# Kernel tuning notes

Hardware: AMD Instinct MI355X
Metric: run time of the kernel (lower is better)

The kernel has to match this reference:

```python
import jax, jax.numpy as jnp
import numpy as np

NUM_NODES = 100000
NUM_EDGES = 1600000
IN_DIM = 128
HID = 128
OUT_DIM = 5


def setup_inputs() -> dict:
    key = jax.random.key(0)
    ks = jax.random.split(key, 8)
    x = jax.random.normal(ks[0], (NUM_NODES, IN_DIM), dtype=jnp.float32)
    edges = jax.random.randint(ks[1], (2, NUM_EDGES), 0, NUM_NODES, dtype=jnp.int32)
    s = 1.0 / np.sqrt(IN_DIM)
    W1 = jax.random.uniform(ks[2], (IN_DIM, HID), jnp.float32, -s, s)
    b1 = jax.random.uniform(ks[3], (HID,), jnp.float32, -s, s)
    sh = 1.0 / np.sqrt(HID)
    W2 = jax.random.uniform(ks[4], (HID, HID), jnp.float32, -sh, sh)
    b2 = jax.random.uniform(ks[5], (HID,), jnp.float32, -sh, sh)
    Wp = jax.random.uniform(ks[6], (HID, OUT_DIM), jnp.float32, -sh, sh)
    bp = jax.random.uniform(ks[7], (OUT_DIM,), jnp.float32, -sh, sh)
    return {"x": x, "edges": edges, "W1": W1, "b1": b1, "W2": W2, "b2": b2, "Wp": Wp, "bp": bp}


def _gnn_layer(x, src, tgt, W, b):
    # scatter-add of source features into targets (mean aggregation)
    agg = jax.ops.segment_sum(x[src], tgt, num_segments=NUM_NODES)  # [N, d]
    cnt = jax.ops.segment_sum(jnp.ones_like(tgt, dtype=x.dtype), tgt, num_segments=NUM_NODES)
    cnt = jnp.maximum(cnt, 1.0)  # clamp(min=1)
    agg = agg / cnt[:, None]
    combined = x + agg  # residual
    return jax.nn.relu(combined @ W + b)


def reference(x, edges, W1, b1, W2, b2, Wp, bp):
    src, tgt = edges[0], edges[1]
    h = _gnn_layer(x, src, tgt, W1, b1)
    h = _gnn_layer(h, src, tgt, W2, b2)
    return h @ Wp + bp  # [N, OUT_DIM]
```

## Files before the change

kernel.cpp:

```cpp
#include <hip/hip_runtime.h>

typedef unsigned int uint32;
typedef unsigned short ushort16;

typedef __attribute__((ext_vector_type(8))) short short8;
typedef __attribute__((ext_vector_type(4))) float f32x4;


#define RSH 11
#define NRG 2048
#define CAP 49152
#define CH  2048

__device__ __forceinline__ ushort16 f2bf(float f) {
    uint32 u = __float_as_uint(f);
    u += 0x7fffu + ((u >> 16) & 1u);
    return (ushort16)(u >> 16);
}
__device__ __forceinline__ float bfhi(uint32 u) { return __uint_as_float(u & 0xffff0000u); }
__device__ __forceinline__ float bflo(uint32 u) { return __uint_as_float(u << 16); }
__device__ __forceinline__ uint32 pack2(float a, float b) {
    return (uint32)f2bf(a) | ((uint32)f2bf(b) << 16);
}

union U16 { uint4 u; short8 s; };
__device__ __forceinline__ short8 ld_frag(const ushort16* p) {
    U16 x; x.u = *(const uint4*)p; return x.s;
}

#define ACC8(v) \
    acc[0] += bflo(v.x); acc[1] += bfhi(v.x); \
    acc[2] += bflo(v.y); acc[3] += bfhi(v.y); \
    acc[4] += bflo(v.z); acc[5] += bfhi(v.z); \
    acc[6] += bflo(v.w); acc[7] += bfhi(v.w);

__global__ __launch_bounds__(256)
void count_prep_kernel(const int* __restrict__ tgt, int* __restrict__ hist,
                       const float* __restrict__ W1, const float* __restrict__ W2,
                       ushort16* __restrict__ Wt1, ushort16* __restrict__ Wt2,
                       int E, int PB, int R) {
    int tid = threadIdx.x, blk = blockIdx.x;
    if (blk >= PB) {
        int idx = blk - PB;
        const float* W = (idx >> 3) ? W2 : W1;
        ushort16* Wt = (idx >> 3) ? Wt2 : Wt1;
        int i0 = (idx & 7) * 2048 + tid * 8;
        float4 a = *(const float4*)(W + i0);
        float4 b = *(const float4*)(W + i0 + 4);
        int k = i0 >> 7, col = i0 & 127;
        Wt[(col + 0) * 128 + k] = f2bf(a.x);
        Wt[(col + 1) * 128 + k] = f2bf(a.y);
        Wt[(col + 2) * 128 + k] = f2bf(a.z);
        Wt[(col + 3) * 128 + k] = f2bf(a.w);
        Wt[(col + 4) * 128 + k] = f2bf(b.x);
        Wt[(col + 5) * 128 + k] = f2bf(b.y);
        Wt[(col + 6) * 128 + k] = f2bf(b.z);
        Wt[(col + 7) * 128 + k] = f2bf(b.w);
        return;
    }
    __shared__ int cnt[64];
    if (tid < 64) cnt[tid] = 0;
    __syncthreads();
    int q0 = blk * (CH / 4), q1 = min(q0 + CH / 4, E / 4);
    for (int q = q0 + tid; q < q1; q += 256) {
        int4 t = ((const int4*)tgt)[q];
        atomicAdd(&cnt[t.x >> RSH], 1);
        atomicAdd(&cnt[t.y >> RSH], 1);
        atomicAdd(&cnt[t.z >> RSH], 1);
        atomicAdd(&cnt[t.w >> RSH], 1);
    }
    __syncthreads();
    if (tid < R) hist[(size_t)blk * 64 + tid] = cnt[tid];
}

__global__ __launch_bounds__(256)
void scan_kernel(int* __restrict__ hist, int* __restrict__ total, int PB) {
    __shared__ int sd[256];
    __shared__ int carrySh;
    int r = blockIdx.x, tid = threadIdx.x;
    if (tid == 0) carrySh = 0;
    __syncthreads();
    int chunks = (PB + 255) >> 8;
    for (int ch = 0; ch < chunks; ++ch) {
        int g = ch * 256 + tid;
        int v = (g < PB) ? hist[(size_t)g * 64 + r] : 0;
        int c0 = carrySh;
        sd[tid] = v;
        __syncthreads();
        for (int o = 1; o < 256; o <<= 1) {
            int t = (tid >= o) ? sd[tid - o] : 0;
            __syncthreads();
            sd[tid] += t;
            __syncthreads();
        }
        if (g < PB) hist[(size_t)g * 64 + r] = sd[tid] - v + c0;
        int tot = sd[255];
        __syncthreads();
        if (tid == 0) carrySh = c0 + tot;
        __syncthreads();
    }
    if (tid == 0) total[r] = carrySh;
}

__global__ __launch_bounds__(256)
void scatter_kernel(const int* __restrict__ src, const int* __restrict__ tgt,
                    const int* __restrict__ hist, uint2* __restrict__ rlist,
                    int E, int R) {
    __shared__ int cb[64];
    __shared__ int cnt[64];
    int tid = threadIdx.x, blk = blockIdx.x;
    if (tid < 64) {
        cnt[tid] = 0;
        cb[tid] = (tid < R) ? hist[(size_t)blk * 64 + tid] : 0;
    }
    __syncthreads();
    int q0 = blk * (CH / 4), q1 = min(q0 + CH / 4, E / 4);
    for (int q = q0 + tid; q < q1; q += 256) {
        int4 t = ((const int4*)tgt)[q];
        int4 s = ((const int4*)src)[q];
        int r0 = t.x >> RSH, r1 = t.y >> RSH, r2 = t.z >> RSH, r3 = t.w >> RSH;
        int l0 = atomicAdd(&cnt[r0], 1);
        int l1 = atomicAdd(&cnt[r1], 1);
        int l2 = atomicAdd(&cnt[r2], 1);
        int l3 = atomicAdd(&cnt[r3], 1);
        int p0 = cb[r0] + l0, p1 = cb[r1] + l1, p2 = cb[r2] + l2, p3 = cb[r3] + l3;
        if (p0 < CAP) rlist[(size_t)r0 * CAP + p0] = make_uint2((uint32)s.x, (uint32)t.x);
        if (p1 < CAP) rlist[(size_t)r1 * CAP + p1] = make_uint2((uint32)s.y, (uint32)t.y);
        if (p2 < CAP) rlist[(size_t)r2 * CAP + p2] = make_uint2((uint32)s.z, (uint32)t.z);
        if (p3 < CAP) rlist[(size_t)r3 * CAP + p3] = make_uint2((uint32)s.w, (uint32)t.w);
    }
}

template<int INF32>
__device__ __forceinline__
void gemm_rows(const void* __restrict__ Asrc, const ushort16* __restrict__ Wt,
               int M, ushort16* __restrict__ outB, int r0w) {
    const int lane = threadIdx.x & 63;
    const int l15 = lane & 15;
    const int quad = lane >> 4;

    int arow = r0w + l15;
    if (arow >= M) arow = M - 1;

    short8 afr[4];
    if (INF32) {
        const float* ap = (const float*)Asrc + (size_t)arow * 128 + quad * 8;
#pragma unroll
        for (int kt = 0; kt < 4; ++kt) {
            float4 a0 = *(const float4*)(ap + kt * 32);
            float4 a1 = *(const float4*)(ap + kt * 32 + 4);
            short8 f;
            f[0] = (short)f2bf(a0.x); f[1] = (short)f2bf(a0.y);
            f[2] = (short)f2bf(a0.z); f[3] = (short)f2bf(a0.w);
            f[4] = (short)f2bf(a1.x); f[5] = (short)f2bf(a1.y);
            f[6] = (short)f2bf(a1.z); f[7] = (short)f2bf(a1.w);
            afr[kt] = f;
        }
    } else {
        const ushort16* aptr = (const ushort16*)Asrc + (size_t)arow * 128 + quad * 8;
#pragma unroll
        for (int kt = 0; kt < 4; ++kt) afr[kt] = ld_frag(aptr + kt * 32);
    }

    f32x4 acc[8];
#pragma unroll
    for (int t = 0; t < 8; ++t) acc[t] = (f32x4){0.f, 0.f, 0.f, 0.f};

#pragma unroll
    for (int t = 0; t < 8; ++t) {
        const ushort16* bptr = Wt + (size_t)(16 * t + l15) * 128 + quad * 8;
        short8 b0 = ld_frag(bptr);
        short8 b1 = ld_frag(bptr + 32);
        short8 b2 = ld_frag(bptr + 64);
        short8 b3 = ld_frag(bptr + 96);
        acc[t] = __builtin_amdgcn_mfma_f32_16x16x32_bf16(afr[0], b0, acc[t], 0, 0, 0);
        acc[t] = __builtin_amdgcn_mfma_f32_16x16x32_bf16(afr[1], b1, acc[t], 0, 0, 0);
        acc[t] = __builtin_amdgcn_mfma_f32_16x16x32_bf16(afr[2], b2, acc[t], 0, 0, 0);
        acc[t] = __builtin_amdgcn_mfma_f32_16x16x32_bf16(afr[3], b3, acc[t], 0, 0, 0);
    }

#pragma unroll
    for (int t = 0; t < 8; ++t) {
        float ov[4];
        ov[0] = acc[t].x; ov[1] = acc[t].y; ov[2] = acc[t].z; ov[3] = acc[t].w;
#pragma unroll
        for (int r = 0; r < 4; ++r) {
            float nb = __shfl_xor(ov[r], 1, 64);
            int row = r0w + quad * 4 + r;
            if (((l15 & 1) == 0) && row < M) {
                *(uint32*)(outB + (size_t)row * 128 + 16 * t + l15) = pack2(ov[r], nb);
            }
        }
    }
}

__global__ __launch_bounds__(1024)
void csr_gemm1_kernel(const uint2* __restrict__ rlist, const int* __restrict__ total,
                      int* __restrict__ start, int* __restrict__ deg,
                      int* __restrict__ csr, int N, int R,
                      const float* __restrict__ x, const ushort16* __restrict__ Wt1,
                      ushort16* __restrict__ ybuf) {
    int blk = blockIdx.x;
    int tid = threadIdx.x;
    if (blk >= R) {
        int gid = blk - R;
        gemm_rows<1>(x, Wt1, N, ybuf, gid * 256 + (tid >> 6) * 16);
        return;
    }
    __shared__ int hist[NRG];
    __shared__ int sd[1024];
    __shared__ int carrySh;
    __shared__ int rbaseSh, countSh;

    int r = blk;
    if (tid == 0) countSh = min(total[r], CAP);
    if (tid < 64) {
        int v = (tid < R) ? total[tid] : 0;
        int pm = (tid < r) ? v : 0;
#pragma unroll
        for (int o = 1; o < 64; o <<= 1) pm += __shfl_xor(pm, o, 64);
        if (tid == 0) rbaseSh = pm;
    }
    for (int i = tid; i < NRG; i += 1024) hist[i] = 0;
    __syncthreads();
    int count = countSh;
    const uint2* rl = rlist + (size_t)r * CAP;
    int n0 = r << RSH;

    {
        int i = tid;
        for (; i + 3072 < count; i += 4096) {
            uint2 a = rl[i], b = rl[i + 1024], c = rl[i + 2048], d = rl[i + 3072];
            atomicAdd(&hist[a.y & (NRG - 1)], 1);
            atomicAdd(&hist[b.y & (NRG - 1)], 1);
            atomicAdd(&hist[c.y & (NRG - 1)], 1);
            atomicAdd(&hist[d.y & (NRG - 1)], 1);
        }
        for (; i < count; i += 1024)
            atomicAdd(&hist[rl[i].y & (NRG - 1)], 1);
    }
    __syncthreads();

    if (tid == 0) carrySh = rbaseSh;
    __syncthreads();
    for (int ch = 0; ch < 2; ++ch) {
        int idx = ch * 1024 + tid;
        int v = hist[idx];
        int c0 = carrySh;
        sd[tid] = v;
        __syncthreads();
        for (int o = 1; o < 1024; o <<= 1) {
            int t = (tid >= o) ? sd[tid - o] : 0;
            __syncthreads();
            sd[tid] += t;
            __syncthreads();
        }
        int excl = sd[tid] - v + c0;
        int tot = sd[1023];
        int node = n0 + idx;
        if (node < N) { start[node] = excl; deg[node] = v; }
        __syncthreads();
        hist[idx] = excl;
        if (tid == 0) carrySh = c0 + tot;
        __syncthreads();
    }

    {
        int i = tid;
        for (; i + 3072 < count; i += 4096) {
            uint2 a = rl[i], b = rl[i + 1024], c = rl[i + 2048], d = rl[i + 3072];
            int pa = atomicAdd(&hist[a.y & (NRG - 1)], 1);
            int pb = atomicAdd(&hist[b.y & (NRG - 1)], 1);
            int pc = atomicAdd(&hist[c.y & (NRG - 1)], 1);
            int pd = atomicAdd(&hist[d.y & (NRG - 1)], 1);
            csr[pa] = (int)a.x;
            csr[pb] = (int)b.x;
            csr[pc] = (int)c.x;
            csr[pd] = (int)d.x;
        }
        for (; i < count; i += 1024) {
            uint2 e = rl[i];
            int p = atomicAdd(&hist[e.y & (NRG - 1)], 1);
            csr[p] = (int)e.x;
        }
    }
}

template<int INF32>
__global__ __launch_bounds__(256)
void gemm_raw_kernel(const void* __restrict__ Asrc, const ushort16* __restrict__ Wt,
                     int M, ushort16* __restrict__ outB) {
    gemm_rows<INF32>(Asrc, Wt, M, outB, blockIdx.x * 64 + (threadIdx.x >> 6) * 16);
}

template<int PROJ>
__global__ __launch_bounds__(256, 4)
void agg_fuse_kernel(const ushort16* __restrict__ hb,
                     const int* __restrict__ start, const int* __restrict__ degv,
                     const int* __restrict__ csr,
                     const float* __restrict__ bias,
                     uint32* __restrict__ outb,
                     const float* __restrict__ Wp, const float* __restrict__ bp,
                     float* __restrict__ outP, int N) {
    int wid = (blockIdx.x * 256 + threadIdx.x) >> 6;
    int lane = threadIdx.x & 63;
    if (wid >= N) return;
    int g = lane >> 4, sl = lane & 15;
    int s0 = start[wid];
    int deg = degv[wid];
    int fi = sl * 4 + g;
    uint32 su = ((const uint32*)hb)[(size_t)wid * 64 + fi];

    float acc[8];
#pragma unroll
    for (int j = 0; j < 8; ++j) acc[j] = 0.f;

    int base = 0;
    for (; base + 8 <= deg; base += 8) {
        int i0 = csr[s0 + base + g];
        int i1 = csr[s0 + base + 4 + g];
        uint4 v0 = *(const uint4*)(hb + (size_t)i0 * 128 + sl * 8);
        uint4 v1 = *(const uint4*)(hb + (size_t)i1 * 128 + sl * 8);
        ACC8(v0); ACC8(v1);
    }
    for (; base < deg; base += 4) {
        int e = base + g;
        if (e < deg) {
            int s = csr[s0 + e];
            uint4 v = *(const uint4*)(hb + (size_t)s * 128 + sl * 8);
            ACC8(v);
        }
    }
#pragma unroll
    for (int j = 0; j < 8; ++j) {
        acc[j] += __shfl_xor(acc[j], 16, 64);
        acc[j] += __shfl_xor(acc[j], 32, 64);
    }
    float inv = 1.f / fmaxf((float)deg, 1.f);
    float ax = (g == 0) ? acc[0] : (g == 1) ? acc[2] : (g == 2) ? acc[4] : acc[6];
    float ay = (g == 0) ? acc[1] : (g == 1) ? acc[3] : (g == 2) ? acc[5] : acc[7];

    float ha = fmaxf(bflo(su) + ax * inv + bias[2 * fi],     0.f);
    float hc = fmaxf(bfhi(su) + ay * inv + bias[2 * fi + 1], 0.f);

    if (!PROJ) {
        outb[(size_t)wid * 64 + fi] = pack2(ha, hc);
    } else {
        float p[5];
#pragma unroll
        for (int j = 0; j < 5; ++j)
            p[j] = ha * Wp[(2 * fi) * 5 + j] + hc * Wp[(2 * fi + 1) * 5 + j];
#pragma unroll
        for (int m = 1; m <= 32; m <<= 1)
#pragma unroll
            for (int j = 0; j < 5; ++j) p[j] += __shfl_xor(p[j], m, 64);
        if (lane == 0) {
#pragma unroll
            for (int j = 0; j < 5; ++j) outP[(size_t)wid * 5 + j] = p[j] + bp[j];
        }
    }
}

extern "C" void kernel_launch(void* const* d_in, const int* in_sizes, int n_in,
                              void* d_out, int out_size, void* d_ws, size_t ws_size,
                              hipStream_t stream) {
    const float* x     = (const float*)d_in[0];
    const int*   edges = (const int*)d_in[1];
    const float* W1    = (const float*)d_in[2];
    const float* b1    = (const float*)d_in[3];
    const float* W2    = (const float*)d_in[4];
    const float* b2    = (const float*)d_in[5];
    const float* Wp    = (const float*)d_in[6];
    const float* bp    = (const float*)d_in[7];
    float* out = (float*)d_out;

    int N = in_sizes[0] / 128;
    int E = in_sizes[1] / 2;
    const int* src = edges;
    const int* tgt = edges + E;

    const int R  = (N + NRG - 1) >> RSH;
    const int PB = (E + CH - 1) / CH;

    char* ws = (char*)d_ws;
    size_t off = 0;
    auto alloc = [&](size_t bytes) {
        char* p = ws + off;
        off = (off + bytes + 255) & ~(size_t)255;
        return p;
    };
    int*      deg     = (int*)alloc((size_t)N * 4);
    int*      start   = (int*)alloc((size_t)N * 4);
    int*      csr     = (int*)alloc((size_t)E * 4);
    uint2*    rlist   = (uint2*)alloc((size_t)R * CAP * 8);
    int*      hist    = (int*)alloc((size_t)PB * 64 * 4);
    int*      total   = (int*)alloc(64 * 4);
    ushort16* ybuf    = (ushort16*)alloc((size_t)N * 128 * 2);
    ushort16* h1      = (ushort16*)alloc((size_t)N * 128 * 2);
    ushort16* Wt1     = (ushort16*)alloc(128 * 128 * 2);
    ushort16* Wt2     = (ushort16*)alloc(128 * 128 * 2);
    (void)ws_size;

    const int g1Blocks   = (N + 255) / 256;
    const int gemmBlocks = (N + 63) / 64;
    const int aggBlocks  = (N + 3) / 4;

    count_prep_kernel<<<PB + 16, 256, 0, stream>>>(tgt, hist, W1, W2, Wt1, Wt2,
                                                   E, PB, R);
    scan_kernel<<<R, 256, 0, stream>>>(hist, total, PB);
    scatter_kernel<<<PB, 256, 0, stream>>>(src, tgt, hist, rlist, E, R);
    csr_gemm1_kernel<<<R + g1Blocks, 1024, 0, stream>>>(rlist, total, start, deg,
                                                        csr, N, R, x, Wt1, ybuf);
    agg_fuse_kernel<0><<<aggBlocks, 256, 0, stream>>>(ybuf, start, deg, csr, b1,
                                                      (uint32*)h1, nullptr, nullptr,
                                                      nullptr, N);
    gemm_raw_kernel<0><<<gemmBlocks, 256, 0, stream>>>(h1, Wt2, N, ybuf);
    agg_fuse_kernel<1><<<aggBlocks, 256, 0, stream>>>(ybuf, start, deg, csr, b2,
                                                      nullptr, Wp, bp, out, N);
}
```

Baseline: 325.3 us.

## Fuse edge partition count/scan/scatter into one kernel with atomic cursors

Replaces the three-kernel partition pipeline (per-block histogram, global scan, scatter) with one kernel. Each block counts its edges in shared memory, reserves space per range through a global atomic cursor, then scatters. This drops two launches and the hist round trip. Bucket ranges shrink to 1024 nodes (up to 128 ranges), so the CSR build now scans one chunk, and nontemporal loads and stores are used throughout. In exchange, edge order inside each range is no longer deterministic, and smaller buckets give more, smaller work units.

```diff
diff --git a/kernel.cpp b/kernel.cpp
--- a/kernel.cpp
+++ b/kernel.cpp
@@ -5,11 +5,14 @@
 
 typedef __attribute__((ext_vector_type(8))) short short8;
 typedef __attribute__((ext_vector_type(4))) float f32x4;
-
-
-#define RSH 11
-#define NRG 2048
-#define CAP 49152
+typedef __attribute__((ext_vector_type(4))) int i32x4;
+typedef __attribute__((ext_vector_type(2))) uint32 u32x2;
+typedef __attribute__((ext_vector_type(4))) uint32 u32x4;
+
+
+#define RSH 10
+#define NRG 1024
+#define CAP 24576
 #define CH  2048
 
 __device__ __forceinline__ ushort16 f2bf(float f) {
@@ -26,6 +29,10 @@
 union U16 { uint4 u; short8 s; };
 __device__ __forceinline__ short8 ld_frag(const ushort16* p) {
     U16 x; x.u = *(const uint4*)p; return x.s;
+}
+union U16NT { u32x4 u; short8 s; };
+__device__ __forceinline__ short8 ld_frag_nt(const ushort16* p) {
+    U16NT x; x.u = __builtin_nontemporal_load((const u32x4*)p); return x.s;
 }
 
 #define ACC8(v) \
@@ -35,10 +42,11 @@
     acc[6] += bflo(v.w); acc[7] += bfhi(v.w);
 
 __global__ __launch_bounds__(256)
-void count_prep_kernel(const int* __restrict__ tgt, int* __restrict__ hist,
-                       const float* __restrict__ W1, const float* __restrict__ W2,
-                       ushort16* __restrict__ Wt1, ushort16* __restrict__ Wt2,
-                       int E, int PB, int R) {
+void partition_prep_kernel(const int* __restrict__ src, const int* __restrict__ tgt,
+                           uint2* __restrict__ rlist, int* __restrict__ rcursor,
+                           const float* __restrict__ W1, const float* __restrict__ W2,
+                           ushort16* __restrict__ Wt1, ushort16* __restrict__ Wt2,
+                           int E, int PB, int R) {
     int tid = threadIdx.x, blk = blockIdx.x;
     if (blk >= PB) {
         int idx = blk - PB;
@@ -58,76 +66,48 @@
         Wt[(col + 7) * 128 + k] = f2bf(b.w);
         return;
     }
-    __shared__ int cnt[64];
-    if (tid < 64) cnt[tid] = 0;
+    __shared__ int cnt[128];
+    __shared__ int cbase[128];
+    if (tid < 128) cnt[tid] = 0;
     __syncthreads();
     int q0 = blk * (CH / 4), q1 = min(q0 + CH / 4, E / 4);
     for (int q = q0 + tid; q < q1; q += 256) {
-        int4 t = ((const int4*)tgt)[q];
+        i32x4 t = __builtin_nontemporal_load((const i32x4*)tgt + q);
         atomicAdd(&cnt[t.x >> RSH], 1);
         atomicAdd(&cnt[t.y >> RSH], 1);
         atomicAdd(&cnt[t.z >> RSH], 1);
         atomicAdd(&cnt[t.w >> RSH], 1);
     }
-    __syncthreads();
-    if (tid < R) hist[(size_t)blk * 64 + tid] = cnt[tid];
-}
-
-__global__ __launch_bounds__(256)
-void scan_kernel(int* __restrict__ hist, int* __restrict__ total, int PB) {
-    __shared__ int sd[256];
-    __shared__ int carrySh;
-    int r = blockIdx.x, tid = threadIdx.x;
-    if (tid == 0) carrySh = 0;
-    __syncthreads();
-    int chunks = (PB + 255) >> 8;
-    for (int ch = 0; ch < chunks; ++ch) {
-        int g = ch * 256 + tid;
-        int v = (g < PB) ? hist[(size_t)g * 64 + r] : 0;
-        int c0 = carrySh;
-        sd[tid] = v;
-        __syncthreads();
-        for (int o = 1; o < 256; o <<= 1) {
-            int t = (tid >= o) ? sd[tid - o] : 0;
-            __syncthreads();
-            sd[tid] += t;
-            __syncthreads();
-        }
-        if (g < PB) hist[(size_t)g * 64 + r] = sd[tid] - v + c0;
-        int tot = sd[255];
-        __syncthreads();
-        if (tid == 0) carrySh = c0 + tot;
-        __syncthreads();
-    }
-    if (tid == 0) total[r] = carrySh;
-}
-
-__global__ __launch_bounds__(256)
-void scatter_kernel(const int* __restrict__ src, const int* __restrict__ tgt,
-                    const int* __restrict__ hist, uint2* __restrict__ rlist,
-                    int E, int R) {
-    __shared__ int cb[64];
-    __shared__ int cnt[64];
-    int tid = threadIdx.x, blk = blockIdx.x;
-    if (tid < 64) {
-        cnt[tid] = 0;
-        cb[tid] = (tid < R) ? hist[(size_t)blk * 64 + tid] : 0;
-    }
-    __syncthreads();
-    int q0 = blk * (CH / 4), q1 = min(q0 + CH / 4, E / 4);
+    if (blk == 0 && tid == 0)
+        for (int e = (E / 4) * 4; e < E; ++e) atomicAdd(&cnt[tgt[e] >> RSH], 1);
+    __syncthreads();
+    if (tid < R) cbase[tid] = atomicAdd(&rcursor[tid], cnt[tid]);
+    __syncthreads();
+    if (tid < 128) cnt[tid] = 0;
+    __syncthreads();
     for (int q = q0 + tid; q < q1; q += 256) {
-        int4 t = ((const int4*)tgt)[q];
-        int4 s = ((const int4*)src)[q];
+        i32x4 t = __builtin_nontemporal_load((const i32x4*)tgt + q);
+        i32x4 s = __builtin_nontemporal_load((const i32x4*)src + q);
         int r0 = t.x >> RSH, r1 = t.y >> RSH, r2 = t.z >> RSH, r3 = t.w >> RSH;
-        int l0 = atomicAdd(&cnt[r0], 1);
-        int l1 = atomicAdd(&cnt[r1], 1);
-        int l2 = atomicAdd(&cnt[r2], 1);
-        int l3 = atomicAdd(&cnt[r3], 1);
-        int p0 = cb[r0] + l0, p1 = cb[r1] + l1, p2 = cb[r2] + l2, p3 = cb[r3] + l3;
-        if (p0 < CAP) rlist[(size_t)r0 * CAP + p0] = make_uint2((uint32)s.x, (uint32)t.x);
-        if (p1 < CAP) rlist[(size_t)r1 * CAP + p1] = make_uint2((uint32)s.y, (uint32)t.y);
-        if (p2 < CAP) rlist[(size_t)r2 * CAP + p2] = make_uint2((uint32)s.z, (uint32)t.z);
-        if (p3 < CAP) rlist[(size_t)r3 * CAP + p3] = make_uint2((uint32)s.w, (uint32)t.w);
+        int p0 = cbase[r0] + atomicAdd(&cnt[r0], 1);
+        int p1 = cbase[r1] + atomicAdd(&cnt[r1], 1);
+        int p2 = cbase[r2] + atomicAdd(&cnt[r2], 1);
+        int p3 = cbase[r3] + atomicAdd(&cnt[r3], 1);
+        u32x2 e0; e0.x = (uint32)s.x; e0.y = (uint32)t.x;
+        u32x2 e1; e1.x = (uint32)s.y; e1.y = (uint32)t.y;
+        u32x2 e2; e2.x = (uint32)s.z; e2.y = (uint32)t.z;
+        u32x2 e3; e3.x = (uint32)s.w; e3.y = (uint32)t.w;
+        if (p0 < CAP) __builtin_nontemporal_store(e0, (u32x2*)&rlist[(size_t)r0 * CAP + p0]);
+        if (p1 < CAP) __builtin_nontemporal_store(e1, (u32x2*)&rlist[(size_t)r1 * CAP + p1]);
+        if (p2 < CAP) __builtin_nontemporal_store(e2, (u32x2*)&rlist[(size_t)r2 * CAP + p2]);
+        if (p3 < CAP) __builtin_nontemporal_store(e3, (u32x2*)&rlist[(size_t)r3 * CAP + p3]);
+    }
+    if (blk == 0 && tid == 0) {
+        for (int e = (E / 4) * 4; e < E; ++e) {
+            int t = tgt[e], r = t >> RSH;
+            int p = cbase[r] + atomicAdd(&cnt[r], 1);
+            if (p < CAP) rlist[(size_t)r * CAP + p] = make_uint2((uint32)src[e], (uint32)t);
+        }
     }
 }
 
@@ -147,8 +127,8 @@
         const float* ap = (const float*)Asrc + (size_t)arow * 128 + quad * 8;
 #pragma unroll
         for (int kt = 0; kt < 4; ++kt) {
-            float4 a0 = *(const float4*)(ap + kt * 32);
-            float4 a1 = *(const float4*)(ap + kt * 32 + 4);
+            f32x4 a0 = __builtin_nontemporal_load((const f32x4*)(ap + kt * 32));
+            f32x4 a1 = __builtin_nontemporal_load((const f32x4*)(ap + kt * 32 + 4));
             short8 f;
             f[0] = (short)f2bf(a0.x); f[1] = (short)f2bf(a0.y);
             f[2] = (short)f2bf(a0.z); f[3] = (short)f2bf(a0.w);
@@ -159,7 +139,7 @@
     } else {
         const ushort16* aptr = (const ushort16*)Asrc + (size_t)arow * 128 + quad * 8;
 #pragma unroll
-        for (int kt = 0; kt < 4; ++kt) afr[kt] = ld_frag(aptr + kt * 32);
+        for (int kt = 0; kt < 4; ++kt) afr[kt] = ld_frag_nt(aptr + kt * 32);
     }
 
     f32x4 acc[8];
@@ -188,14 +168,15 @@
             float nb = __shfl_xor(ov[r], 1, 64);
             int row = r0w + quad * 4 + r;
             if (((l15 & 1) == 0) && row < M) {
-                *(uint32*)(outB + (size_t)row * 128 + 16 * t + l15) = pack2(ov[r], nb);
+                __builtin_nontemporal_store(pack2(ov[r], nb),
+                    (uint32*)(outB + (size_t)row * 128 + 16 * t + l15));
             }
         }
     }
 }
 
 __global__ __launch_bounds__(1024)
-void csr_gemm1_kernel(const uint2* __restrict__ rlist, const int* __restrict__ total,
+void csr_gemm1_kernel(const uint2* __restrict__ rlist, const int* __restrict__ rcursor,
                       int* __restrict__ start, int* __restrict__ deg,
                       int* __restrict__ csr, int N, int R,
                       const float* __restrict__ x, const ushort16* __restrict__ Wt1,
@@ -209,44 +190,50 @@
     }
     __shared__ int hist[NRG];
     __shared__ int sd[1024];
-    __shared__ int carrySh;
     __shared__ int rbaseSh, countSh;
 
     int r = blk;
-    if (tid == 0) countSh = min(total[r], CAP);
-    if (tid < 64) {
-        int v = (tid < R) ? total[tid] : 0;
-        int pm = (tid < r) ? v : 0;
-#pragma unroll
-        for (int o = 1; o < 64; o <<= 1) pm += __shfl_xor(pm, o, 64);
-        if (tid == 0) rbaseSh = pm;
-    }
-    for (int i = tid; i < NRG; i += 1024) hist[i] = 0;
+    if (tid < 128) sd[tid] = (tid < R) ? rcursor[tid] : 0;
+    __syncthreads();
+    for (int o = 1; o < 128; o <<= 1) {
+        int t = (tid >= o && tid < 128) ? sd[tid - o] : 0;
+        __syncthreads();
+        if (tid < 128) sd[tid] += t;
+        __syncthreads();
+    }
+    if (tid == 0) {
+        int incl = sd[r];
+        int excl = (r == 0) ? 0 : sd[r - 1];
+        rbaseSh = excl;
+        countSh = min(incl - excl, CAP);
+    }
+    hist[tid] = 0;
     __syncthreads();
     int count = countSh;
-    const uint2* rl = rlist + (size_t)r * CAP;
+    const u32x2* rl = (const u32x2*)(rlist + (size_t)r * CAP);
     int n0 = r << RSH;
 
     {
         int i = tid;
         for (; i + 3072 < count; i += 4096) {
-            uint2 a = rl[i], b = rl[i + 1024], c = rl[i + 2048], d = rl[i + 3072];
+            u32x2 a = __builtin_nontemporal_load(rl + i);
+            u32x2 b = __builtin_nontemporal_load(rl + i + 1024);
+            u32x2 c = __builtin_nontemporal_load(rl + i + 2048);
+            u32x2 d = __builtin_nontemporal_load(rl + i + 3072);
             atomicAdd(&hist[a.y & (NRG - 1)], 1);
             atomicAdd(&hist[b.y & (NRG - 1)], 1);
             atomicAdd(&hist[c.y & (NRG - 1)], 1);
             atomicAdd(&hist[d.y & (NRG - 1)], 1);
         }
-        for (; i < count; i += 1024)
-            atomicAdd(&hist[rl[i].y & (NRG - 1)], 1);
-    }
-    __syncthreads();
-
-    if (tid == 0) carrySh = rbaseSh;
-    __syncthreads();
-    for (int ch = 0; ch < 2; ++ch) {
-        int idx = ch * 1024 + tid;
-        int v = hist[idx];
-        int c0 = carrySh;
+        for (; i < count; i += 1024) {
+            u32x2 e = __builtin_nontemporal_load(rl + i);
+            atomicAdd(&hist[e.y & (NRG - 1)], 1);
+        }
+    }
+    __syncthreads();
+
+    {
+        int v = hist[tid];
         sd[tid] = v;
         __syncthreads();
         for (int o = 1; o < 1024; o <<= 1) {
@@ -255,33 +242,33 @@
             sd[tid] += t;
             __syncthreads();
         }
-        int excl = sd[tid] - v + c0;
-        int tot = sd[1023];
-        int node = n0 + idx;
+        int excl = sd[tid] - v + rbaseSh;
+        int node = n0 + tid;
         if (node < N) { start[node] = excl; deg[node] = v; }
-        __syncthreads();
-        hist[idx] = excl;
-        if (tid == 0) carrySh = c0 + tot;
+        hist[tid] = excl;
         __syncthreads();
     }
 
     {
         int i = tid;
         for (; i + 3072 < count; i += 4096) {
-            uint2 a = rl[i], b = rl[i + 1024], c = rl[i + 2048], d = rl[i + 3072];
+            u32x2 a = __builtin_nontemporal_load(rl + i);
+            u32x2 b = __builtin_nontemporal_load(rl + i + 1024);
+            u32x2 c = __builtin_nontemporal_load(rl + i + 2048);
+            u32x2 d = __builtin_nontemporal_load(rl + i + 3072);
             int pa = atomicAdd(&hist[a.y & (NRG - 1)], 1);
             int pb = atomicAdd(&hist[b.y & (NRG - 1)], 1);
             int pc = atomicAdd(&hist[c.y & (NRG - 1)], 1);
             int pd = atomicAdd(&hist[d.y & (NRG - 1)], 1);
-            csr[pa] = (int)a.x;
-            csr[pb] = (int)b.x;
-            csr[pc] = (int)c.x;
-            csr[pd] = (int)d.x;
+            __builtin_nontemporal_store((int)a.x, &csr[pa]);
+            __builtin_nontemporal_store((int)b.x, &csr[pb]);
+            __builtin_nontemporal_store((int)c.x, &csr[pc]);
+            __builtin_nontemporal_store((int)d.x, &csr[pd]);
         }
         for (; i < count; i += 1024) {
-            uint2 e = rl[i];
+            u32x2 e = __builtin_nontemporal_load(rl + i);
             int p = atomicAdd(&hist[e.y & (NRG - 1)], 1);
-            csr[p] = (int)e.x;
+            __builtin_nontemporal_store((int)e.x, &csr[p]);
         }
     }
 }
@@ -344,7 +331,7 @@
     float hc = fmaxf(bfhi(su) + ay * inv + bias[2 * fi + 1], 0.f);
 
     if (!PROJ) {
-        outb[(size_t)wid * 64 + fi] = pack2(ha, hc);
+        __builtin_nontemporal_store(pack2(ha, hc), &outb[(size_t)wid * 64 + fi]);
     } else {
         float p[5];
 #pragma unroll
@@ -356,7 +343,8 @@
             for (int j = 0; j < 5; ++j) p[j] += __shfl_xor(p[j], m, 64);
         if (lane == 0) {
 #pragma unroll
-            for (int j = 0; j < 5; ++j) outP[(size_t)wid * 5 + j] = p[j] + bp[j];
+            for (int j = 0; j < 5; ++j)
+                __builtin_nontemporal_store(p[j] + bp[j], &outP[(size_t)wid * 5 + j]);
         }
     }
 }
@@ -393,8 +381,7 @@
     int*      start   = (int*)alloc((size_t)N * 4);
     int*      csr     = (int*)alloc((size_t)E * 4);
     uint2*    rlist   = (uint2*)alloc((size_t)R * CAP * 8);
-    int*      hist    = (int*)alloc((size_t)PB * 64 * 4);
-    int*      total   = (int*)alloc(64 * 4);
+    int*      rcursor = (int*)alloc(128 * 4);
     ushort16* ybuf    = (ushort16*)alloc((size_t)N * 128 * 2);
     ushort16* h1      = (ushort16*)alloc((size_t)N * 128 * 2);
     ushort16* Wt1     = (ushort16*)alloc(128 * 128 * 2);
@@ -405,11 +392,10 @@
     const int gemmBlocks = (N + 63) / 64;
     const int aggBlocks  = (N + 3) / 4;
 
-    count_prep_kernel<<<PB + 16, 256, 0, stream>>>(tgt, hist, W1, W2, Wt1, Wt2,
-                                                   E, PB, R);
-    scan_kernel<<<R, 256, 0, stream>>>(hist, total, PB);
-    scatter_kernel<<<PB, 256, 0, stream>>>(src, tgt, hist, rlist, E, R);
-    csr_gemm1_kernel<<<R + g1Blocks, 1024, 0, stream>>>(rlist, total, start, deg,
+    (void)hipMemsetAsync(rcursor, 0, 128 * 4, stream);
+    partition_prep_kernel<<<PB + 16, 256, 0, stream>>>(src, tgt, rlist, rcursor,
+                                                       W1, W2, Wt1, Wt2, E, PB, R);
+    csr_gemm1_kernel<<<R + g1Blocks, 1024, 0, stream>>>(rlist, rcursor, start, deg,
                                                         csr, N, R, x, Wt1, ybuf);
     agg_fuse_kernel<0><<<aggBlocks, 256, 0, stream>>>(ybuf, start, deg, csr, b1,
                                                       (uint32*)h1, nullptr, nullptr,
```

New measurement: 412.8 us. 1.27x slower.

## Move bias+ReLU into next GEMM and split projection into separate kernel

Applied to the files above, without the earlier changes.

The aggregation kernel now only writes the bf16 residual-plus-mean sum, without bias, ReLU or projection. Layer-1 bias and ReLU are applied while loading A fragments in the second GEMM, and a new per-node projection kernel applies layer-2 bias, ReLU and the 128x5 projection, reading Wp from shared memory. This removes the cross-lane shuffle reductions from the aggregation, at the cost of one extra launch and an extra N×128 bf16 read/write. The change also adds tail handling for edge counts not divisible by four and moves rlist to the end of the workspace.

```diff
diff --git a/kernel.cpp b/kernel.cpp
--- a/kernel.cpp
+++ b/kernel.cpp
@@ -69,6 +69,8 @@
         atomicAdd(&cnt[t.z >> RSH], 1);
         atomicAdd(&cnt[t.w >> RSH], 1);
     }
+    if (blk == 0 && tid == 0)
+        for (int e = (E / 4) * 4; e < E; ++e) atomicAdd(&cnt[tgt[e] >> RSH], 1);
     __syncthreads();
     if (tid < R) hist[(size_t)blk * 64 + tid] = cnt[tid];
 }
@@ -119,22 +121,29 @@
         int4 t = ((const int4*)tgt)[q];
         int4 s = ((const int4*)src)[q];
         int r0 = t.x >> RSH, r1 = t.y >> RSH, r2 = t.z >> RSH, r3 = t.w >> RSH;
-        int l0 = atomicAdd(&cnt[r0], 1);
-        int l1 = atomicAdd(&cnt[r1], 1);
-        int l2 = atomicAdd(&cnt[r2], 1);
-        int l3 = atomicAdd(&cnt[r3], 1);
-        int p0 = cb[r0] + l0, p1 = cb[r1] + l1, p2 = cb[r2] + l2, p3 = cb[r3] + l3;
+        int p0 = cb[r0] + atomicAdd(&cnt[r0], 1);
+        int p1 = cb[r1] + atomicAdd(&cnt[r1], 1);
+        int p2 = cb[r2] + atomicAdd(&cnt[r2], 1);
+        int p3 = cb[r3] + atomicAdd(&cnt[r3], 1);
         if (p0 < CAP) rlist[(size_t)r0 * CAP + p0] = make_uint2((uint32)s.x, (uint32)t.x);
         if (p1 < CAP) rlist[(size_t)r1 * CAP + p1] = make_uint2((uint32)s.y, (uint32)t.y);
         if (p2 < CAP) rlist[(size_t)r2 * CAP + p2] = make_uint2((uint32)s.z, (uint32)t.z);
         if (p3 < CAP) rlist[(size_t)r3 * CAP + p3] = make_uint2((uint32)s.w, (uint32)t.w);
     }
-}
-
-template<int INF32>
+    if (blk == 0 && tid == 0) {
+        for (int e = (E / 4) * 4; e < E; ++e) {
+            int t = tgt[e], r = t >> RSH;
+            int p = cb[r] + atomicAdd(&cnt[r], 1);
+            if (p < CAP) rlist[(size_t)r * CAP + p] = make_uint2((uint32)src[e], (uint32)t);
+        }
+    }
+}
+
+template<int MODE>
 __device__ __forceinline__
 void gemm_rows(const void* __restrict__ Asrc, const ushort16* __restrict__ Wt,
-               int M, ushort16* __restrict__ outB, int r0w) {
+               const float* __restrict__ bias, int M,
+               ushort16* __restrict__ outB, int r0w) {
     const int lane = threadIdx.x & 63;
     const int l15 = lane & 15;
     const int quad = lane >> 4;
@@ -143,7 +152,7 @@
     if (arow >= M) arow = M - 1;
 
     short8 afr[4];
-    if (INF32) {
+    if (MODE == 1) {
         const float* ap = (const float*)Asrc + (size_t)arow * 128 + quad * 8;
 #pragma unroll
         for (int kt = 0; kt < 4; ++kt) {
@@ -155,6 +164,21 @@
             f[4] = (short)f2bf(a1.x); f[5] = (short)f2bf(a1.y);
             f[6] = (short)f2bf(a1.z); f[7] = (short)f2bf(a1.w);
             afr[kt] = f;
+        }
+    } else if (MODE == 2) {
+        const ushort16* aptr = (const ushort16*)Asrc + (size_t)arow * 128 + quad * 8;
+#pragma unroll
+        for (int kt = 0; kt < 4; ++kt) {
+            uint4 v = *(const uint4*)(aptr + kt * 32);
+            const float* bb = bias + kt * 32 + quad * 8;
+            float4 b0 = *(const float4*)bb;
+            float4 b1 = *(const float4*)(bb + 4);
+            uint32 w0 = pack2(fmaxf(bflo(v.x) + b0.x, 0.f), fmaxf(bfhi(v.x) + b0.y, 0.f));
+            uint32 w1 = pack2(fmaxf(bflo(v.y) + b0.z, 0.f), fmaxf(bfhi(v.y) + b0.w, 0.f));
+            uint32 w2 = pack2(fmaxf(bflo(v.z) + b1.x, 0.f), fmaxf(bfhi(v.z) + b1.y, 0.f));
+            uint32 w3 = pack2(fmaxf(bflo(v.w) + b1.z, 0.f), fmaxf(bfhi(v.w) + b1.w, 0.f));
+            U16 u; u.u = make_uint4(w0, w1, w2, w3);
+            afr[kt] = u.s;
         }
     } else {
         const ushort16* aptr = (const ushort16*)Asrc + (size_t)arow * 128 + quad * 8;
@@ -204,7 +228,7 @@
     int tid = threadIdx.x;
     if (blk >= R) {
         int gid = blk - R;
-        gemm_rows<1>(x, Wt1, N, ybuf, gid * 256 + (tid >> 6) * 16);
+        gemm_rows<1>(x, Wt1, nullptr, N, ybuf, gid * 256 + (tid >> 6) * 16);
         return;
     }
     __shared__ int hist[NRG];
@@ -286,27 +310,23 @@
     }
 }
 
-template<int INF32>
 __global__ __launch_bounds__(256)
-void gemm_raw_kernel(const void* __restrict__ Asrc, const ushort16* __restrict__ Wt,
-                     int M, ushort16* __restrict__ outB) {
-    gemm_rows<INF32>(Asrc, Wt, M, outB, blockIdx.x * 64 + (threadIdx.x >> 6) * 16);
-}
-
-template<int PROJ>
+void gemm_biasrelu_kernel(const ushort16* __restrict__ A, const ushort16* __restrict__ Wt,
+                          const float* __restrict__ bias, int M,
+                          ushort16* __restrict__ outB) {
+    gemm_rows<2>(A, Wt, bias, M, outB, blockIdx.x * 64 + ((threadIdx.x >> 6)) * 16);
+}
+
 __global__ __launch_bounds__(256, 4)
-void agg_fuse_kernel(const ushort16* __restrict__ hb,
-                     const int* __restrict__ start, const int* __restrict__ degv,
-                     const int* __restrict__ csr,
-                     const float* __restrict__ bias,
-                     uint32* __restrict__ outb,
-                     const float* __restrict__ Wp, const float* __restrict__ bp,
-                     float* __restrict__ outP, int N) {
+void agg_combine_bf16_kernel(const ushort16* __restrict__ hb,
+                             const int* __restrict__ startv, const int* __restrict__ degv,
+                             const int* __restrict__ csr,
+                             uint32* __restrict__ outb, int N) {
     int wid = (blockIdx.x * 256 + threadIdx.x) >> 6;
     int lane = threadIdx.x & 63;
     if (wid >= N) return;
     int g = lane >> 4, sl = lane & 15;
-    int s0 = start[wid];
+    int s0 = startv[wid];
     int deg = degv[wid];
     int fi = sl * 4 + g;
     uint32 su = ((const uint32*)hb)[(size_t)wid * 64 + fi];
@@ -339,26 +359,46 @@
     float inv = 1.f / fmaxf((float)deg, 1.f);
     float ax = (g == 0) ? acc[0] : (g == 1) ? acc[2] : (g == 2) ? acc[4] : acc[6];
     float ay = (g == 0) ? acc[1] : (g == 1) ? acc[3] : (g == 2) ? acc[5] : acc[7];
-
-    float ha = fmaxf(bflo(su) + ax * inv + bias[2 * fi],     0.f);
-    float hc = fmaxf(bfhi(su) + ay * inv + bias[2 * fi + 1], 0.f);
-
-    if (!PROJ) {
-        outb[(size_t)wid * 64 + fi] = pack2(ha, hc);
-    } else {
-        float p[5];
-#pragma unroll
-        for (int j = 0; j < 5; ++j)
-            p[j] = ha * Wp[(2 * fi) * 5 + j] + hc * Wp[(2 * fi + 1) * 5 + j];
-#pragma unroll
-        for (int m = 1; m <= 32; m <<= 1)
-#pragma unroll
-            for (int j = 0; j < 5; ++j) p[j] += __shfl_xor(p[j], m, 64);
-        if (lane == 0) {
-#pragma unroll
-            for (int j = 0; j < 5; ++j) outP[(size_t)wid * 5 + j] = p[j] + bp[j];
-        }
-    }
+    outb[(size_t)wid * 64 + fi] = pack2(bflo(su) + ax * inv, bfhi(su) + ay * inv);
+}
+
+__global__ __launch_bounds__(256)
+void proj_kernel(const ushort16* __restrict__ w, const float* __restrict__ b2,
+                 const float* __restrict__ Wp, const float* __restrict__ bp,
+                 float* __restrict__ out, int N) {
+    __shared__ float wps[640];
+    __shared__ float b2s[128];
+    int tid = threadIdx.x;
+    for (int i = tid; i < 640; i += 256) wps[i] = Wp[i];
+    if (tid < 128) b2s[tid] = b2[tid];
+    __syncthreads();
+    int n = blockIdx.x * 256 + tid;
+    if (n >= N) return;
+    const uint4* row = (const uint4*)(w + (size_t)n * 128);
+    float p0 = 0.f, p1 = 0.f, p2 = 0.f, p3 = 0.f, p4 = 0.f;
+#pragma unroll
+    for (int q = 0; q < 16; ++q) {
+        uint4 v = row[q];
+        int c = q * 8;
+        uint32 ww[4] = {v.x, v.y, v.z, v.w};
+#pragma unroll
+        for (int k = 0; k < 4; ++k) {
+            float hlo = fmaxf(bflo(ww[k]) + b2s[c + 2 * k],     0.f);
+            float hhi = fmaxf(bfhi(ww[k]) + b2s[c + 2 * k + 1], 0.f);
+            const float* wl = &wps[(c + 2 * k) * 5];
+            p0 += hlo * wl[0] + hhi * wl[5];
+            p1 += hlo * wl[1] + hhi * wl[6];
+            p2 += hlo * wl[2] + hhi * wl[7];
+            p3 += hlo * wl[3] + hhi * wl[8];
+            p4 += hlo * wl[4] + hhi * wl[9];
+        }
+    }
+    float* o = out + (size_t)n * 5;
+    o[0] = p0 + bp[0];
+    o[1] = p1 + bp[1];
+    o[2] = p2 + bp[2];
+    o[3] = p3 + bp[3];
+    o[4] = p4 + bp[4];
 }
 
 extern "C" void kernel_launch(void* const* d_in, const int* in_sizes, int n_in,
@@ -392,18 +432,19 @@
     int*      deg     = (int*)alloc((size_t)N * 4);
     int*      start   = (int*)alloc((size_t)N * 4);
     int*      csr     = (int*)alloc((size_t)E * 4);
-    uint2*    rlist   = (uint2*)alloc((size_t)R * CAP * 8);
     int*      hist    = (int*)alloc((size_t)PB * 64 * 4);
     int*      total   = (int*)alloc(64 * 4);
     ushort16* ybuf    = (ushort16*)alloc((size_t)N * 128 * 2);
-    ushort16* h1      = (ushort16*)alloc((size_t)N * 128 * 2);
+    ushort16* abuf    = (ushort16*)alloc((size_t)N * 128 * 2);
     ushort16* Wt1     = (ushort16*)alloc(128 * 128 * 2);
     ushort16* Wt2     = (ushort16*)alloc(128 * 128 * 2);
+    uint2*    rlist   = (uint2*)alloc((size_t)R * CAP * 8);
     (void)ws_size;
 
     const int g1Blocks   = (N + 255) / 256;
     const int gemmBlocks = (N + 63) / 64;
     const int aggBlocks  = (N + 3) / 4;
+    const int projBlocks = (N + 255) / 256;
 
     count_prep_kernel<<<PB + 16, 256, 0, stream>>>(tgt, hist, W1, W2, Wt1, Wt2,
                                                    E, PB, R);
@@ -411,10 +452,10 @@
     scatter_kernel<<<PB, 256, 0, stream>>>(src, tgt, hist, rlist, E, R);
     csr_gemm1_kernel<<<R + g1Blocks, 1024, 0, stream>>>(rlist, total, start, deg,
                                                         csr, N, R, x, Wt1, ybuf);
-    agg_fuse_kernel<0><<<aggBlocks, 256, 0, stream>>>(ybuf, start, deg, csr, b1,
-                                                      (uint32*)h1, nullptr, nullptr,
-                                                      nullptr, N);
-    gemm_raw_kernel<0><<<gemmBlocks, 256, 0, stream>>>(h1, Wt2, N, ybuf);
-    agg_fuse_kernel<1><<<aggBlocks, 256, 0, stream>>>(ybuf, start, deg, csr, b2,
-                                                      nullptr, Wp, bp, out, N);
-}
+    agg_combine_bf16_kernel<<<aggBlocks, 256, 0, stream>>>(ybuf, start, deg, csr,
+                                                           (uint32*)abuf, N);
+    gemm_biasrelu_kernel<<<gemmBlocks, 256, 0, stream>>>(abuf, Wt2, b1, N, ybuf);
+    agg_combine_bf16_kernel<<<aggBlocks, 256, 0, stream>>>(ybuf, start, deg, csr,
+                                                           (uint32*)abuf, N);
+    proj_kernel<<<projBlocks, 256, 0, stream>>>(abuf, b2, Wp, bp, out, N);
+}
```

Result: no change. 329.6 us (+1.3%).
